# Performance work log

Hardware: AMD Instinct MI355X
Metric: run time of the kernel (lower is better)

The kernel has to match this reference:

```python
import jax, jax.numpy as jnp
import numpy as np

N_NODES = 50000
N_EDGES = 500000
IN_FEATS = 64
HIDDEN = 64
OUT_FEATS = 8
N_LAYERS = 6
NEG_SLOPE = 0.2
LN_EPS = 1e-5


def setup_inputs() -> dict:
    key = jax.random.key(0)
    ks = jax.random.split(key, 12)
    s_in = 1.0 / np.sqrt(IN_FEATS)
    s_h = 1.0 / np.sqrt(HIDDEN)
    return {
        "nodes": jax.random.normal(ks[0], (N_NODES, IN_FEATS), jnp.float32),
        "src": jax.random.randint(ks[1], (N_EDGES,), 0, N_NODES, jnp.int32),
        "dst": jax.random.randint(ks[2], (N_EDGES,), 0, N_NODES, jnp.int32),
        "w_in": jax.random.normal(ks[3], (IN_FEATS, HIDDEN), jnp.float32) * s_in,
        "b_in": jnp.zeros((HIDDEN,), jnp.float32),
        "w_src": jax.random.normal(ks[4], (N_LAYERS, HIDDEN, HIDDEN), jnp.float32) * s_h,
        "b_src": jnp.zeros((N_LAYERS, HIDDEN), jnp.float32),
        "w_dst": jax.random.normal(ks[5], (N_LAYERS, HIDDEN, HIDDEN), jnp.float32) * s_h,
        "b_dst": jnp.zeros((N_LAYERS, HIDDEN), jnp.float32),
        "attn": jax.random.normal(ks[6], (N_LAYERS, HIDDEN), jnp.float32) * s_h,
        "gamma": jnp.ones((N_LAYERS, HIDDEN), jnp.float32),
        "beta": jnp.zeros((N_LAYERS, HIDDEN), jnp.float32),
        "w_out": jax.random.normal(ks[7], (HIDDEN, OUT_FEATS), jnp.float32) * s_h,
        "b_out": jnp.zeros((OUT_FEATS,), jnp.float32),
    }


def _layernorm(x, g, b):
    m = jnp.mean(x, axis=-1, keepdims=True)
    v = jnp.mean(jnp.square(x - m), axis=-1, keepdims=True)
    return (x - m) * jax.lax.rsqrt(v + LN_EPS) * g + b


def _gatv2(h, src, dst, ws, bs, wd, bd, a, n_nodes):
    # GATv2Conv, num_heads=1 (DGL semantics)
    fs = h @ ws + bs                                  # [N, H] fc_src
    fd = h @ wd + bd                                  # [N, H] fc_dst
    e = jax.nn.leaky_relu(fs[src] + fd[dst], NEG_SLOPE)  # [E, H]
    score = e @ a                                     # [E]
    # segment softmax over incoming edges of each dst node
    mx = jax.ops.segment_max(score, dst, num_segments=n_nodes)
    ex = jnp.exp(score - mx[dst])
    denom = jax.ops.segment_sum(ex, dst, num_segments=n_nodes)
    alpha = ex / denom[dst]                           # [E]
    return jax.ops.segment_sum(alpha[:, None] * fs[src], dst, num_segments=n_nodes)


def reference(nodes, src, dst, w_in, b_in, w_src, b_src, w_dst, b_dst, attn, gamma, beta, w_out, b_out):
    n = nodes.shape[0]
    h = nodes @ w_in + b_in
    for i in range(N_LAYERS):
        t = _gatv2(h, src, dst, w_src[i], b_src[i], w_dst[i], b_dst[i], attn[i], n)
        t = _layernorm(t, gamma[i], beta[i])
        h = h + jax.nn.gelu(t, approximate=False)
    return h @ w_out + b_out
```

## Files before the change

kernel.cpp:

```cpp
#include <hip/hip_runtime.h>
#include <math.h>

#define N_NODES 50000
#define N_EDGES 500000
#define NLAYERS 6
#define NEG_SLOPE 0.2f
#define LN_EPS 1e-5f
#define SCAN_B 1024
#define NSCAN_BLOCKS ((N_NODES + SCAN_B - 1) / SCAN_B)
#define LOG2E 1.4426950408889634f

typedef __attribute__((ext_vector_type(8))) short short8;
typedef __attribute__((ext_vector_type(4))) float f32x4;

__device__ __forceinline__ float wave_sum64(float v) {
#pragma unroll
    for (int m = 32; m >= 1; m >>= 1) v += __shfl_xor(v, m, 64);
    return v;
}

__device__ __forceinline__ int wave_incl_scan(int v, int lane) {
#pragma unroll
    for (int offs = 1; offs < 64; offs <<= 1) {
        int t = __shfl_up(v, offs, 64);
        if (lane >= offs) v += t;
    }
    return v;
}

__device__ __forceinline__ unsigned bf16_rne(float v) {
    unsigned u = __float_as_uint(v);
    return (u + 0x7fffu + ((u >> 16) & 1u)) >> 16;
}

__device__ __forceinline__ float fast_exp2(float x) {
    float r;
    asm("v_exp_f32 %0, %1" : "=v"(r) : "v"(x));
    return r;
}

__device__ __forceinline__ float4 bf4_to_f4(ushort4 u) {
    float4 r;
    r.x = __uint_as_float((unsigned)u.x << 16);
    r.y = __uint_as_float((unsigned)u.y << 16);
    r.z = __uint_as_float((unsigned)u.z << 16);
    r.w = __uint_as_float((unsigned)u.w << 16);
    return r;
}

__global__ void count_deg(const int* __restrict__ dst, int* __restrict__ deg,
                          int* __restrict__ hist) {
    if (blockIdx.x == 0 && threadIdx.x < 64) hist[threadIdx.x] = 0;
    int i = blockIdx.x * blockDim.x + threadIdx.x;
    if (i < N_EDGES) atomicAdd(&deg[dst[i]], 1);
}

__global__ void histo(const int* __restrict__ deg, int* __restrict__ hist) {
    __shared__ int lhist[64];
    int t = threadIdx.x;
    if (t < 64) lhist[t] = 0;
    __syncthreads();
    int i = blockIdx.x * SCAN_B + t;
    if (i < N_NODES) atomicAdd(&lhist[min(deg[i], 63)], 1);
    __syncthreads();
    if (t < 64) atomicAdd(&hist[t], lhist[t]);
}

__global__ void binscan(const int* __restrict__ hist, int* __restrict__ binpos) {
    int lane = threadIdx.x;
    int v = hist[lane];
    int incl = wave_incl_scan(v, lane);
    binpos[lane] = incl - v;
}

__global__ void bucket_nodes(const int* __restrict__ deg, int* __restrict__ binpos,
                             int* __restrict__ perm, int* __restrict__ inv_perm) {
    __shared__ int lhist[64], lbase[64];
    int t = threadIdx.x;
    if (t < 64) lhist[t] = 0;
    __syncthreads();
    int i = blockIdx.x * SCAN_B + t;
    int b = 0;
    if (i < N_NODES) {
        b = min(deg[i], 63);
        atomicAdd(&lhist[b], 1);
    }
    __syncthreads();
    if (t < 64) {
        lbase[t] = atomicAdd(&binpos[t], lhist[t]);
        lhist[t] = 0;
    }
    __syncthreads();
    if (i < N_NODES) {
        int r = atomicAdd(&lhist[b], 1);
        int p = lbase[b] + r;
        perm[p] = i;
        inv_perm[i] = p;
    }
}

__global__ void scan1p(const int* __restrict__ deg, const int* __restrict__ perm,
                       int* __restrict__ row_ptr_p, int* __restrict__ bsum) {
    __shared__ int wtot[16];
    int t = threadIdx.x;
    int i = blockIdx.x * SCAN_B + t;
    int lane = t & 63, wv = t >> 6;
    int v = (i < N_NODES) ? deg[perm[i]] : 0;
    int incl = wave_incl_scan(v, lane);
    if (lane == 63) wtot[wv] = incl;
    __syncthreads();
    if (wv == 0) {
        int wval = (lane < 16) ? wtot[lane] : 0;
        int ws = wave_incl_scan(wval, lane);
        if (lane < 16) wtot[lane] = ws - wval;
    }
    __syncthreads();
    int excl = incl - v + wtot[wv];
    if (i < N_NODES) row_ptr_p[i] = excl;
    if (t == SCAN_B - 1) bsum[blockIdx.x] = excl + v;
}

__global__ void scan3p(int* __restrict__ row_ptr_p, const int* __restrict__ bsum,
                       int* __restrict__ pos_p) {
    __shared__ int boff_s;
    int t = threadIdx.x;
    if (t < 64) {
        int v = (t < NSCAN_BLOCKS && t < (int)blockIdx.x) ? bsum[t] : 0;
#pragma unroll
        for (int m = 32; m >= 1; m >>= 1) v += __shfl_xor(v, m, 64);
        if (t == 0) boff_s = v;
    }
    __syncthreads();
    int i = blockIdx.x * SCAN_B + t;
    if (i < N_NODES) {
        int r = row_ptr_p[i] + boff_s;
        row_ptr_p[i] = r;
        pos_p[i] = r;
    }
    if (i == 0) row_ptr_p[N_NODES] = N_EDGES;
}

__global__ void scatter_edges(const int* __restrict__ dst, const int* __restrict__ src,
                              const int* __restrict__ inv_perm, int* __restrict__ pos_p,
                              int* __restrict__ srcs_p) {
    int i = blockIdx.x * blockDim.x + threadIdx.x;
    if (i < N_EDGES) {
        int dp = inv_perm[dst[i]];
        int p = atomicAdd(&pos_p[dp], 1);
        srcs_p[p] = inv_perm[src[i]];
    }
}

__global__ void pack_w(const float* __restrict__ w_in, const float* __restrict__ w_src,
                       const float* __restrict__ w_dst, unsigned short* __restrict__ wpk_hi,
                       unsigned short* __restrict__ wpk_lo) {
    int b = blockIdx.x;
    const float* W = (b == 0) ? w_in
                              : (b <= 6 ? w_src + (size_t)(b - 1) * 4096
                                        : w_dst + (size_t)(b - 7) * 4096);
    unsigned short* hi = wpk_hi + (size_t)b * 4096;
    unsigned short* lo = wpk_lo + (size_t)b * 4096;
    for (int idx = threadIdx.x; idx < 4096; idx += 256) {
        int t = idx >> 10;
        int s = (idx >> 9) & 1;
        int l = (idx >> 3) & 63;
        int j = idx & 7;
        int row = s * 32 + (l >> 4) * 8 + j;
        int col = t * 16 + (l & 15);
        float v = W[row * 64 + col];
        unsigned rh = bf16_rne(v);
        float hf = __uint_as_float(rh << 16);
        unsigned rl = bf16_rne(v - hf);
        hi[idx] = (unsigned short)rh;
        lo[idx] = (unsigned short)rl;
    }
}

__device__ __forceinline__ void load_split8(const float* __restrict__ p, short8& hi, short8& lo) {
    float4 x0 = *(const float4*)p;
    float4 x1 = *(const float4*)(p + 4);
    float v[8] = {x0.x, x0.y, x0.z, x0.w, x1.x, x1.y, x1.z, x1.w};
#pragma unroll
    for (int j = 0; j < 8; ++j) {
        unsigned rh = bf16_rne(v[j]);
        float hf = __uint_as_float(rh << 16);
        unsigned rl = bf16_rne(v[j] - hf);
        hi[j] = (short)rh;
        lo[j] = (short)rl;
    }
}

__device__ __forceinline__ void mfma_16rows(const short8 ah0, const short8 ah1, const short8 al0,
                                            const short8 al1,
                                            const unsigned short* __restrict__ whi,
                                            const unsigned short* __restrict__ wlo, int lane,
                                            f32x4 acc[4]) {
#pragma unroll
    for (int t = 0; t < 4; ++t) {
#pragma unroll
        for (int s = 0; s < 2; ++s) {
            const size_t boff = ((size_t)((t * 2 + s) * 64 + lane)) * 8;
            short8 bh = *(const short8*)(whi + boff);
            short8 bl = *(const short8*)(wlo + boff);
            short8 a_h = s ? ah1 : ah0;
            short8 a_l = s ? al1 : al0;
            acc[t] = __builtin_amdgcn_mfma_f32_16x16x32_bf16(a_h, bh, acc[t], 0, 0, 0);
            acc[t] = __builtin_amdgcn_mfma_f32_16x16x32_bf16(a_l, bh, acc[t], 0, 0, 0);
            acc[t] = __builtin_amdgcn_mfma_f32_16x16x32_bf16(a_h, bl, acc[t], 0, 0, 0);
        }
    }
}

__global__ void mfma_in_proj(const float* __restrict__ X, const int* __restrict__ perm,
                             const unsigned short* __restrict__ whi,
                             const unsigned short* __restrict__ wlo,
                             const float* __restrict__ bias, float* __restrict__ H) {
    int lane = threadIdx.x & 63, wv = threadIdx.x >> 6;
    int R = blockIdx.x * 64 + wv * 16;
    int arow = perm[min(R + (lane & 15), N_NODES - 1)];
    const float* p = X + (size_t)arow * 64 + (lane >> 4) * 8;
    short8 ah0, ah1, al0, al1;
    load_split8(p, ah0, al0);
    load_split8(p + 32, ah1, al1);
    f32x4 acc[4];
    f32x4 z = {0.f, 0.f, 0.f, 0.f};
#pragma unroll
    for (int t = 0; t < 4; ++t) acc[t] = z;
    mfma_16rows(ah0, ah1, al0, al1, whi, wlo, lane, acc);
    int crow = R + (lane >> 4) * 4;
#pragma unroll
    for (int t = 0; t < 4; ++t) {
        int col = t * 16 + (lane & 15);
        float bv = bias[col];
#pragma unroll
        for (int r = 0; r < 4; ++r) {
            int row = crow + r;
            if (row < N_NODES) H[(size_t)row * 64 + col] = acc[t][r] + bv;
        }
    }
}

__global__ void mfma_dual(const float* __restrict__ X, const unsigned short* __restrict__ wshi,
                          const unsigned short* __restrict__ wslo, const float* __restrict__ bs,
                          const unsigned short* __restrict__ wdhi,
                          const unsigned short* __restrict__ wdlo, const float* __restrict__ bd,
                          unsigned short* __restrict__ FS, float* __restrict__ FD) {
    int lane = threadIdx.x & 63, wv = threadIdx.x >> 6;
    int R = blockIdx.x * 64 + wv * 16;
    int arow = min(R + (lane & 15), N_NODES - 1);
    const float* p = X + (size_t)arow * 64 + (lane >> 4) * 8;
    short8 ah0, ah1, al0, al1;
    load_split8(p, ah0, al0);
    load_split8(p + 32, ah1, al1);
    f32x4 accS[4], accD[4];
    f32x4 z = {0.f, 0.f, 0.f, 0.f};
#pragma unroll
    for (int t = 0; t < 4; ++t) {
        accS[t] = z;
        accD[t] = z;
    }
    mfma_16rows(ah0, ah1, al0, al1, wshi, wslo, lane, accS);
    mfma_16rows(ah0, ah1, al0, al1, wdhi, wdlo, lane, accD);
    int crow = R + (lane >> 4) * 4;
#pragma unroll
    for (int t = 0; t < 4; ++t) {
        int col = t * 16 + (lane & 15);
        float bsv = bs[col], bdv = bd[col];
#pragma unroll
        for (int r = 0; r < 4; ++r) {
            int row = crow + r;
            if (row < N_NODES) {
                FS[(size_t)row * 64 + col] = (unsigned short)bf16_rne(accS[t][r] + bsv);
                FD[(size_t)row * 64 + col] = accD[t][r] + bdv;
            }
        }
    }
}

#define WPB 4
__global__ void node_fused_kernel(const unsigned short* __restrict__ fs,
                                  const float* __restrict__ fd, const int* __restrict__ row_ptr,
                                  const int* __restrict__ srcs, const float* __restrict__ attn,
                                  const float* __restrict__ gamma, const float* __restrict__ beta,
                                  float* __restrict__ h) {
    __shared__ float xpose[WPB][64];
    int lane = threadIdx.x & 63;
    int wv = threadIdx.x >> 6;
    int q = lane >> 4;
    int ql = lane & 15;
    int f0 = ql << 2;
    int n = blockIdx.x * WPB + wv;
    if (n >= N_NODES) return;
    float gL = gamma[lane], bL = beta[lane];
    float hval = h[(size_t)n * 64 + lane];
    float4 a4 = *(const float4*)&attn[f0];
    a4.x *= LOG2E;
    a4.y *= LOG2E;
    a4.z *= LOG2E;
    a4.w *= LOG2E;
    int beg = row_ptr[n], end = row_ptr[n + 1];
    int deg = end - beg;
    float4 fd4 = *(const float4*)&fd[(size_t)n * 64 + f0];
    float d = 0.f;
    float4 acc = make_float4(0.f, 0.f, 0.f, 0.f);
    for (int c0 = 0; c0 < deg; c0 += 64) {
        int cl = min(64, deg - c0);
        int sv = (lane < cl) ? srcs[beg + c0 + lane] : 0;
        int nt = (cl + 3) >> 2;
        ushort4 rowA = make_ushort4(0, 0, 0, 0), rowB = rowA;
        int sid0 = __shfl(sv, q, 64);
        if (q < cl) rowA = *(const ushort4*)&fs[(size_t)sid0 * 64 + f0];
        int sid1 = __shfl(sv, (4 + q) & 63, 64);
        if (4 + q < cl) rowB = *(const ushort4*)&fs[(size_t)sid1 * 64 + f0];
        for (int t = 0; t < nt; ++t) {
            int eoff = 4 * t + q;
            bool valid = eoff < cl;
            float4 cur = bf4_to_f4(rowA);
            rowA = rowB;
            int e2 = 4 * (t + 2) + q;
            int sid2 = __shfl(sv, e2 & 63, 64);
            if (e2 < cl) rowB = *(const ushort4*)&fs[(size_t)sid2 * 64 + f0];
            float vx = cur.x + fd4.x, vy = cur.y + fd4.y;
            float vz = cur.z + fd4.z, vw = cur.w + fd4.w;
            vx = fmaxf(vx, NEG_SLOPE * vx);
            vy = fmaxf(vy, NEG_SLOPE * vy);
            vz = fmaxf(vz, NEG_SLOPE * vz);
            vw = fmaxf(vw, NEG_SLOPE * vw);
            float sp = fmaf(a4.x, vx, fmaf(a4.y, vy, fmaf(a4.z, vz, a4.w * vw)));
            sp += __shfl_xor(sp, 1, 64);
            sp += __shfl_xor(sp, 2, 64);
            sp += __shfl_xor(sp, 4, 64);
            sp += __shfl_xor(sp, 8, 64);
            float w = valid ? fast_exp2(sp) : 0.f;
            d += w;
            acc.x = fmaf(w, cur.x, acc.x);
            acc.y = fmaf(w, cur.y, acc.y);
            acc.z = fmaf(w, cur.z, acc.z);
            acc.w = fmaf(w, cur.w, acc.w);
        }
    }
    d += __shfl_xor(d, 16, 64);
    d += __shfl_xor(d, 32, 64);
    acc.x += __shfl_xor(acc.x, 16, 64);
    acc.y += __shfl_xor(acc.y, 16, 64);
    acc.z += __shfl_xor(acc.z, 16, 64);
    acc.w += __shfl_xor(acc.w, 16, 64);
    acc.x += __shfl_xor(acc.x, 32, 64);
    acc.y += __shfl_xor(acc.y, 32, 64);
    acc.z += __shfl_xor(acc.z, 32, 64);
    acc.w += __shfl_xor(acc.w, 32, 64);
    float inv = (d > 0.f) ? 1.f / d : 0.f;
    acc.x *= inv;
    acc.y *= inv;
    acc.z *= inv;
    acc.w *= inv;
    if (q == 0) *(float4*)&xpose[wv][f0] = acc;
    float val = xpose[wv][lane];
    float mean = wave_sum64(val) * 0.015625f;
    float dev = val - mean;
    float var = wave_sum64(dev * dev) * 0.015625f;
    float rstd = rsqrtf(var + LN_EPS);
    float tval = fmaf(dev * rstd, gL, bL);
    float g = 0.5f * tval * (1.f + erff(tval * 0.70710678118654752f));
    h[(size_t)n * 64 + lane] = hval + g;
}

__global__ void out_proj_kernel(const float* __restrict__ h, const int* __restrict__ perm,
                                const float* __restrict__ W, const float* __restrict__ b,
                                float* __restrict__ out) {
    __shared__ float Ws[64 * 8];
    __shared__ float bs[8];
    __shared__ float Hs[32][65];
    int t = threadIdx.x;
    for (int i = t; i < 512; i += 256) Ws[i] = W[i];
    if (t < 8) bs[t] = b[t];
    int n0 = blockIdx.x * 32;
    for (int i = t; i < 32 * 64; i += 256) {
        int r = i >> 6, c = i & 63;
        int n = n0 + r;
        Hs[r][c] = (n < N_NODES) ? h[(size_t)n * 64 + c] : 0.f;
    }
    __syncthreads();
    int nl = t >> 3, o = t & 7;
    int n = n0 + nl;
    if (n >= N_NODES) return;
    float acc = bs[o];
#pragma unroll
    for (int k = 0; k < 64; ++k) acc = fmaf(Hs[nl][k], Ws[k * 8 + o], acc);
    out[(size_t)perm[n] * 8 + o] = acc;
}

extern "C" void kernel_launch(void* const* d_in, const int* in_sizes, int n_in,
                              void* d_out, int out_size, void* d_ws, size_t ws_size,
                              hipStream_t stream) {
    const float* nodes = (const float*)d_in[0];
    const int* src = (const int*)d_in[1];
    const int* dst = (const int*)d_in[2];
    const float* w_in = (const float*)d_in[3];
    const float* b_in = (const float*)d_in[4];
    const float* w_src = (const float*)d_in[5];
    const float* b_src = (const float*)d_in[6];
    const float* w_dst = (const float*)d_in[7];
    const float* b_dst = (const float*)d_in[8];
    const float* attn = (const float*)d_in[9];
    const float* gamma = (const float*)d_in[10];
    const float* beta = (const float*)d_in[11];
    const float* w_out = (const float*)d_in[12];
    const float* b_out = (const float*)d_in[13];
    float* out = (float*)d_out;

    char* ws = (char*)d_ws;
    size_t off = 0;
    auto alloc = [&](size_t bytes) {
        void* p = ws + off;
        off += (bytes + 255) & ~(size_t)255;
        return p;
    };
    float* h = (float*)alloc((size_t)N_NODES * 64 * 4);
    unsigned short* fs = (unsigned short*)alloc((size_t)N_NODES * 64 * 2);
    float* fd = (float*)alloc((size_t)N_NODES * 64 * 4);
    unsigned short* wpk_hi = (unsigned short*)alloc((size_t)13 * 4096 * 2);
    unsigned short* wpk_lo = (unsigned short*)alloc((size_t)13 * 4096 * 2);
    int* deg = (int*)alloc((size_t)N_NODES * 4);
    int* row_ptr_p = (int*)alloc((size_t)(N_NODES + 1) * 4);
    int* pos_p = (int*)alloc((size_t)N_NODES * 4);
    int* srcs_p = (int*)alloc((size_t)N_EDGES * 4);
    int* bsum = (int*)alloc((size_t)NSCAN_BLOCKS * 4);
    int* hist = (int*)alloc((size_t)64 * 4);
    int* binpos = (int*)alloc((size_t)64 * 4);
    int* perm = (int*)alloc((size_t)N_NODES * 4);
    int* inv_perm = (int*)alloc((size_t)N_NODES * 4);

    hipMemsetAsync(deg, 0, (size_t)N_NODES * 4, stream);
    count_deg<<<(N_EDGES + 255) / 256, 256, 0, stream>>>(dst, deg, hist);
    histo<<<NSCAN_BLOCKS, SCAN_B, 0, stream>>>(deg, hist);
    binscan<<<1, 64, 0, stream>>>(hist, binpos);
    bucket_nodes<<<NSCAN_BLOCKS, SCAN_B, 0, stream>>>(deg, binpos, perm, inv_perm);
    scan1p<<<NSCAN_BLOCKS, SCAN_B, 0, stream>>>(deg, perm, row_ptr_p, bsum);
    scan3p<<<NSCAN_BLOCKS, SCAN_B, 0, stream>>>(row_ptr_p, bsum, pos_p);
    scatter_edges<<<(N_EDGES + 255) / 256, 256, 0, stream>>>(dst, src, inv_perm, pos_p, srcs_p);

    pack_w<<<13, 256, 0, stream>>>(w_in, w_src, w_dst, wpk_hi, wpk_lo);

    mfma_in_proj<<<(N_NODES + 63) / 64, 256, 0, stream>>>(nodes, perm, wpk_hi, wpk_lo, b_in, h);

    for (int l = 0; l < NLAYERS; ++l) {
        mfma_dual<<<(N_NODES + 63) / 64, 256, 0, stream>>>(
            h, wpk_hi + (size_t)(1 + l) * 4096, wpk_lo + (size_t)(1 + l) * 4096,
            b_src + (size_t)l * 64, wpk_hi + (size_t)(7 + l) * 4096,
            wpk_lo + (size_t)(7 + l) * 4096, b_dst + (size_t)l * 64, fs, fd);
        node_fused_kernel<<<(N_NODES + WPB - 1) / WPB, 256, 0, stream>>>(
            fs, fd, row_ptr_p, srcs_p, attn + (size_t)l * 64, gamma + (size_t)l * 64,
            beta + (size_t)l * 64, h);
    }

    out_proj_kernel<<<(N_NODES + 31) / 32, 256, 0, stream>>>(h, perm, w_out, b_out, out);
}
```

Before: 346.7 us.

## Fuse graph preprocessing kernels into one cooperative grid-synced kernel

Replaces the memset, degree count, histogram, bucket sort, two-pass scan, edge scatter and weight packing kernels with a single cooperative kernel. Phases are separated by grid-wide syncs and the per-element loops become grid-stride loops over a 49-block grid. This is meant to remove several kernel launches and the idle gaps between them. In exchange, the edge-wide atomic phases run with fewer threads and every phase pays for a grid barrier.

```diff
diff --git a/kernel.cpp b/kernel.cpp
--- a/kernel.cpp
+++ b/kernel.cpp
@@ -1,5 +1,8 @@
 #include <hip/hip_runtime.h>
+#include <hip/hip_cooperative_groups.h>
 #include <math.h>
+
+namespace cg = cooperative_groups;
 
 #define N_NODES 50000
 #define N_EDGES 500000
@@ -48,131 +51,119 @@
     return r;
 }
 
-__global__ void count_deg(const int* __restrict__ dst, int* __restrict__ deg,
-                          int* __restrict__ hist) {
-    if (blockIdx.x == 0 && threadIdx.x < 64) hist[threadIdx.x] = 0;
-    int i = blockIdx.x * blockDim.x + threadIdx.x;
-    if (i < N_EDGES) atomicAdd(&deg[dst[i]], 1);
-}
-
-__global__ void histo(const int* __restrict__ deg, int* __restrict__ hist) {
-    __shared__ int lhist[64];
-    int t = threadIdx.x;
-    if (t < 64) lhist[t] = 0;
-    __syncthreads();
-    int i = blockIdx.x * SCAN_B + t;
-    if (i < N_NODES) atomicAdd(&lhist[min(deg[i], 63)], 1);
-    __syncthreads();
-    if (t < 64) atomicAdd(&hist[t], lhist[t]);
-}
-
-__global__ void binscan(const int* __restrict__ hist, int* __restrict__ binpos) {
-    int lane = threadIdx.x;
-    int v = hist[lane];
-    int incl = wave_incl_scan(v, lane);
-    binpos[lane] = incl - v;
-}
-
-__global__ void bucket_nodes(const int* __restrict__ deg, int* __restrict__ binpos,
-                             int* __restrict__ perm, int* __restrict__ inv_perm) {
-    __shared__ int lhist[64], lbase[64];
-    int t = threadIdx.x;
-    if (t < 64) lhist[t] = 0;
-    __syncthreads();
-    int i = blockIdx.x * SCAN_B + t;
-    int b = 0;
-    if (i < N_NODES) {
-        b = min(deg[i], 63);
-        atomicAdd(&lhist[b], 1);
-    }
-    __syncthreads();
-    if (t < 64) {
-        lbase[t] = atomicAdd(&binpos[t], lhist[t]);
-        lhist[t] = 0;
-    }
-    __syncthreads();
-    if (i < N_NODES) {
-        int r = atomicAdd(&lhist[b], 1);
-        int p = lbase[b] + r;
-        perm[p] = i;
-        inv_perm[i] = p;
-    }
-}
-
-__global__ void scan1p(const int* __restrict__ deg, const int* __restrict__ perm,
-                       int* __restrict__ row_ptr_p, int* __restrict__ bsum) {
-    __shared__ int wtot[16];
-    int t = threadIdx.x;
-    int i = blockIdx.x * SCAN_B + t;
-    int lane = t & 63, wv = t >> 6;
-    int v = (i < N_NODES) ? deg[perm[i]] : 0;
-    int incl = wave_incl_scan(v, lane);
-    if (lane == 63) wtot[wv] = incl;
-    __syncthreads();
-    if (wv == 0) {
-        int wval = (lane < 16) ? wtot[lane] : 0;
-        int ws = wave_incl_scan(wval, lane);
-        if (lane < 16) wtot[lane] = ws - wval;
-    }
-    __syncthreads();
-    int excl = incl - v + wtot[wv];
-    if (i < N_NODES) row_ptr_p[i] = excl;
-    if (t == SCAN_B - 1) bsum[blockIdx.x] = excl + v;
-}
-
-__global__ void scan3p(int* __restrict__ row_ptr_p, const int* __restrict__ bsum,
-                       int* __restrict__ pos_p) {
+__global__ void __launch_bounds__(SCAN_B) build_all(
+    const int* __restrict__ dst, const int* __restrict__ src, const float* __restrict__ w_in,
+    const float* __restrict__ w_src, const float* __restrict__ w_dst,
+    unsigned short* __restrict__ wpk_hi, unsigned short* __restrict__ wpk_lo,
+    int* __restrict__ deg, int* __restrict__ hist, int* __restrict__ binpos,
+    int* __restrict__ perm, int* __restrict__ inv_perm, int* __restrict__ row_ptr_p,
+    int* __restrict__ pos_p, int* __restrict__ srcs_p, int* __restrict__ bsum) {
+    cg::grid_group grid = cg::this_grid();
+    __shared__ int lhist[64], lbase[64], wtot[16];
     __shared__ int boff_s;
-    int t = threadIdx.x;
-    if (t < 64) {
-        int v = (t < NSCAN_BLOCKS && t < (int)blockIdx.x) ? bsum[t] : 0;
-#pragma unroll
-        for (int m = 32; m >= 1; m >>= 1) v += __shfl_xor(v, m, 64);
-        if (t == 0) boff_s = v;
-    }
-    __syncthreads();
-    int i = blockIdx.x * SCAN_B + t;
-    if (i < N_NODES) {
-        int r = row_ptr_p[i] + boff_s;
-        row_ptr_p[i] = r;
-        pos_p[i] = r;
-    }
-    if (i == 0) row_ptr_p[N_NODES] = N_EDGES;
-}
-
-__global__ void scatter_edges(const int* __restrict__ dst, const int* __restrict__ src,
-                              const int* __restrict__ inv_perm, int* __restrict__ pos_p,
-                              int* __restrict__ srcs_p) {
-    int i = blockIdx.x * blockDim.x + threadIdx.x;
-    if (i < N_EDGES) {
-        int dp = inv_perm[dst[i]];
-        int p = atomicAdd(&pos_p[dp], 1);
-        srcs_p[p] = inv_perm[src[i]];
-    }
-}
-
-__global__ void pack_w(const float* __restrict__ w_in, const float* __restrict__ w_src,
-                       const float* __restrict__ w_dst, unsigned short* __restrict__ wpk_hi,
-                       unsigned short* __restrict__ wpk_lo) {
-    int b = blockIdx.x;
-    const float* W = (b == 0) ? w_in
-                              : (b <= 6 ? w_src + (size_t)(b - 1) * 4096
-                                        : w_dst + (size_t)(b - 7) * 4096);
-    unsigned short* hi = wpk_hi + (size_t)b * 4096;
-    unsigned short* lo = wpk_lo + (size_t)b * 4096;
-    for (int idx = threadIdx.x; idx < 4096; idx += 256) {
-        int t = idx >> 10;
-        int s = (idx >> 9) & 1;
-        int l = (idx >> 3) & 63;
-        int j = idx & 7;
+    const int t = threadIdx.x;
+    const int bid = blockIdx.x;
+    const int gtid = bid * SCAN_B + t;
+    const int GSZ = NSCAN_BLOCKS * SCAN_B;
+
+    for (int i = gtid; i < N_NODES; i += GSZ) deg[i] = 0;
+    if (gtid < 64) hist[gtid] = 0;
+    for (int idx = gtid; idx < 13 * 4096; idx += GSZ) {
+        int b = idx >> 12;
+        int k = idx & 4095;
+        const float* W = (b == 0) ? w_in
+                                  : (b <= 6 ? w_src + (size_t)(b - 1) * 4096
+                                            : w_dst + (size_t)(b - 7) * 4096);
+        int tt = k >> 10;
+        int s = (k >> 9) & 1;
+        int l = (k >> 3) & 63;
+        int j = k & 7;
         int row = s * 32 + (l >> 4) * 8 + j;
-        int col = t * 16 + (l & 15);
+        int col = tt * 16 + (l & 15);
         float v = W[row * 64 + col];
         unsigned rh = bf16_rne(v);
         float hf = __uint_as_float(rh << 16);
         unsigned rl = bf16_rne(v - hf);
-        hi[idx] = (unsigned short)rh;
-        lo[idx] = (unsigned short)rl;
+        wpk_hi[(size_t)b * 4096 + k] = (unsigned short)rh;
+        wpk_lo[(size_t)b * 4096 + k] = (unsigned short)rl;
+    }
+    grid.sync();
+
+    for (int i = gtid; i < N_EDGES; i += GSZ) atomicAdd(&deg[dst[i]], 1);
+    grid.sync();
+
+    if (t < 64) lhist[t] = 0;
+    __syncthreads();
+    if (gtid < N_NODES) atomicAdd(&lhist[min(deg[gtid], 63)], 1);
+    __syncthreads();
+    if (t < 64) atomicAdd(&hist[t], lhist[t]);
+    grid.sync();
+
+    if (bid == 0 && t < 64) {
+        int v = hist[t];
+        int incl = wave_incl_scan(v, t);
+        binpos[t] = incl - v;
+    }
+    grid.sync();
+
+    if (t < 64) lhist[t] = 0;
+    __syncthreads();
+    int bkt = 0;
+    if (gtid < N_NODES) {
+        bkt = min(deg[gtid], 63);
+        atomicAdd(&lhist[bkt], 1);
+    }
+    __syncthreads();
+    if (t < 64) {
+        lbase[t] = atomicAdd(&binpos[t], lhist[t]);
+        lhist[t] = 0;
+    }
+    __syncthreads();
+    if (gtid < N_NODES) {
+        int r = atomicAdd(&lhist[bkt], 1);
+        int p = lbase[bkt] + r;
+        perm[p] = gtid;
+        inv_perm[gtid] = p;
+    }
+    grid.sync();
+
+    {
+        int lane = t & 63, wv = t >> 6;
+        int v = (gtid < N_NODES) ? deg[perm[gtid]] : 0;
+        int incl = wave_incl_scan(v, lane);
+        if (lane == 63) wtot[wv] = incl;
+        __syncthreads();
+        if (wv == 0) {
+            int wval = (lane < 16) ? wtot[lane] : 0;
+            int ws = wave_incl_scan(wval, lane);
+            if (lane < 16) wtot[lane] = ws - wval;
+        }
+        __syncthreads();
+        int excl = incl - v + wtot[wv];
+        if (gtid < N_NODES) row_ptr_p[gtid] = excl;
+        if (t == SCAN_B - 1) bsum[bid] = excl + v;
+    }
+    grid.sync();
+
+    if (t < 64) {
+        int v = (t < NSCAN_BLOCKS && t < bid) ? bsum[t] : 0;
+#pragma unroll
+        for (int m = 32; m >= 1; m >>= 1) v += __shfl_xor(v, m, 64);
+        if (t == 0) boff_s = v;
+    }
+    __syncthreads();
+    if (gtid < N_NODES) {
+        int r = row_ptr_p[gtid] + boff_s;
+        row_ptr_p[gtid] = r;
+        pos_p[gtid] = r;
+    }
+    if (gtid == 0) row_ptr_p[N_NODES] = N_EDGES;
+    grid.sync();
+
+    for (int i = gtid; i < N_EDGES; i += GSZ) {
+        int dp = inv_perm[dst[i]];
+        int p = atomicAdd(&pos_p[dp], 1);
+        srcs_p[p] = inv_perm[src[i]];
     }
 }
 
@@ -431,16 +422,14 @@
     int* perm = (int*)alloc((size_t)N_NODES * 4);
     int* inv_perm = (int*)alloc((size_t)N_NODES * 4);
 
-    hipMemsetAsync(deg, 0, (size_t)N_NODES * 4, stream);
-    count_deg<<<(N_EDGES + 255) / 256, 256, 0, stream>>>(dst, deg, hist);
-    histo<<<NSCAN_BLOCKS, SCAN_B, 0, stream>>>(deg, hist);
-    binscan<<<1, 64, 0, stream>>>(hist, binpos);
-    bucket_nodes<<<NSCAN_BLOCKS, SCAN_B, 0, stream>>>(deg, binpos, perm, inv_perm);
-    scan1p<<<NSCAN_BLOCKS, SCAN_B, 0, stream>>>(deg, perm, row_ptr_p, bsum);
-    scan3p<<<NSCAN_BLOCKS, SCAN_B, 0, stream>>>(row_ptr_p, bsum, pos_p);
-    scatter_edges<<<(N_EDGES + 255) / 256, 256, 0, stream>>>(dst, src, inv_perm, pos_p, srcs_p);
-
-    pack_w<<<13, 256, 0, stream>>>(w_in, w_src, w_dst, wpk_hi, wpk_lo);
+    {
+        void* args[] = {(void*)&dst,    (void*)&src,    (void*)&w_in,     (void*)&w_src,
+                        (void*)&w_dst,  (void*)&wpk_hi, (void*)&wpk_lo,   (void*)&deg,
+                        (void*)&hist,   (void*)&binpos, (void*)&perm,     (void*)&inv_perm,
+                        (void*)&row_ptr_p, (void*)&pos_p, (void*)&srcs_p, (void*)&bsum};
+        hipLaunchCooperativeKernel((const void*)build_all, dim3(NSCAN_BLOCKS), dim3(SCAN_B),
+                                   args, 0, stream);
+    }
 
     mfma_in_proj<<<(N_NODES + 63) / 64, 256, 0, stream>>>(nodes, perm, wpk_hi, wpk_lo, b_in, h);
 
```

New measurement: 419.8 us. +21.1%, slower.

## Fuse next-layer src/dst projections into node kernel and input projection

Applied to the files above, without the earlier changes.

Removes the separate per-layer mfma_dual kernel. The input projection now also computes layer-0 FS/FD through a shared-memory transpose. Each node_fused_kernel wave computes the next layer's FS/FD for its single node using MFMA with 15 of 16 rows zeroed, writing into double-buffered fs/fd arrays. This cuts six kernel launches and the re-read of h, at the cost of heavily wasted MFMA work (one useful row per 16) and extra register pressure in the gather kernel.

```diff
diff --git a/kernel.cpp b/kernel.cpp
--- a/kernel.cpp
+++ b/kernel.cpp
@@ -176,7 +176,7 @@
     }
 }
 
-__device__ __forceinline__ void load_split8(const float* __restrict__ p, short8& hi, short8& lo) {
+__device__ __forceinline__ void load_split8(const float* p, short8& hi, short8& lo) {
     float4 x0 = *(const float4*)p;
     float4 x1 = *(const float4*)(p + 4);
     float v[8] = {x0.x, x0.y, x0.z, x0.w, x1.x, x1.y, x1.z, x1.w};
@@ -214,7 +214,15 @@
 __global__ void mfma_in_proj(const float* __restrict__ X, const int* __restrict__ perm,
                              const unsigned short* __restrict__ whi,
                              const unsigned short* __restrict__ wlo,
-                             const float* __restrict__ bias, float* __restrict__ H) {
+                             const float* __restrict__ bias, float* __restrict__ H,
+                             const unsigned short* __restrict__ wshi,
+                             const unsigned short* __restrict__ wslo,
+                             const float* __restrict__ bs,
+                             const unsigned short* __restrict__ wdhi,
+                             const unsigned short* __restrict__ wdlo,
+                             const float* __restrict__ bd, unsigned short* __restrict__ FS,
+                             float* __restrict__ FD) {
+    __shared__ float tr[4][16 * 64];
     int lane = threadIdx.x & 63, wv = threadIdx.x >> 6;
     int R = blockIdx.x * 64 + wv * 16;
     int arow = perm[min(R + (lane & 15), N_NODES - 1)];
@@ -228,6 +236,7 @@
     for (int t = 0; t < 4; ++t) acc[t] = z;
     mfma_16rows(ah0, ah1, al0, al1, whi, wlo, lane, acc);
     int crow = R + (lane >> 4) * 4;
+    int lrow0 = (lane >> 4) * 4;
 #pragma unroll
     for (int t = 0; t < 4; ++t) {
         int col = t * 16 + (lane & 15);
@@ -235,25 +244,14 @@
 #pragma unroll
         for (int r = 0; r < 4; ++r) {
             int row = crow + r;
-            if (row < N_NODES) H[(size_t)row * 64 + col] = acc[t][r] + bv;
-        }
-    }
-}
-
-__global__ void mfma_dual(const float* __restrict__ X, const unsigned short* __restrict__ wshi,
-                          const unsigned short* __restrict__ wslo, const float* __restrict__ bs,
-                          const unsigned short* __restrict__ wdhi,
-                          const unsigned short* __restrict__ wdlo, const float* __restrict__ bd,
-                          unsigned short* __restrict__ FS, float* __restrict__ FD) {
-    int lane = threadIdx.x & 63, wv = threadIdx.x >> 6;
-    int R = blockIdx.x * 64 + wv * 16;
-    int arow = min(R + (lane & 15), N_NODES - 1);
-    const float* p = X + (size_t)arow * 64 + (lane >> 4) * 8;
-    short8 ah0, ah1, al0, al1;
-    load_split8(p, ah0, al0);
-    load_split8(p + 32, ah1, al1);
+            float v = acc[t][r] + bv;
+            if (row < N_NODES) H[(size_t)row * 64 + col] = v;
+            tr[wv][(lrow0 + r) * 64 + col] = v;
+        }
+    }
+    load_split8(&tr[wv][(lane & 15) * 64 + (lane >> 4) * 8], ah0, al0);
+    load_split8(&tr[wv][(lane & 15) * 64 + 32 + (lane >> 4) * 8], ah1, al1);
     f32x4 accS[4], accD[4];
-    f32x4 z = {0.f, 0.f, 0.f, 0.f};
 #pragma unroll
     for (int t = 0; t < 4; ++t) {
         accS[t] = z;
@@ -261,7 +259,6 @@
     }
     mfma_16rows(ah0, ah1, al0, al1, wshi, wslo, lane, accS);
     mfma_16rows(ah0, ah1, al0, al1, wdhi, wdlo, lane, accD);
-    int crow = R + (lane >> 4) * 4;
 #pragma unroll
     for (int t = 0; t < 4; ++t) {
         int col = t * 16 + (lane & 15);
@@ -282,7 +279,14 @@
                                   const float* __restrict__ fd, const int* __restrict__ row_ptr,
                                   const int* __restrict__ srcs, const float* __restrict__ attn,
                                   const float* __restrict__ gamma, const float* __restrict__ beta,
-                                  float* __restrict__ h) {
+                                  float* __restrict__ h,
+                                  const unsigned short* __restrict__ nws_hi,
+                                  const unsigned short* __restrict__ nws_lo,
+                                  const float* __restrict__ nbs,
+                                  const unsigned short* __restrict__ nwd_hi,
+                                  const unsigned short* __restrict__ nwd_lo,
+                                  const float* __restrict__ nbd,
+                                  unsigned short* __restrict__ nFS, float* __restrict__ nFD) {
     __shared__ float xpose[WPB][64];
     int lane = threadIdx.x & 63;
     int wv = threadIdx.x >> 6;
@@ -362,7 +366,38 @@
     float rstd = rsqrtf(var + LN_EPS);
     float tval = fmaf(dev * rstd, gL, bL);
     float g = 0.5f * tval * (1.f + erff(tval * 0.70710678118654752f));
-    h[(size_t)n * 64 + lane] = hval + g;
+    float hnew = hval + g;
+    h[(size_t)n * 64 + lane] = hnew;
+    if (nws_hi) {
+        xpose[wv][lane] = hnew;
+        short8 ah0, ah1, al0, al1;
+        load_split8(&xpose[wv][(lane >> 4) * 8], ah0, al0);
+        load_split8(&xpose[wv][32 + (lane >> 4) * 8], ah1, al1);
+        if (lane & 15) {
+            const short8 s8z = {0, 0, 0, 0, 0, 0, 0, 0};
+            ah0 = s8z;
+            ah1 = s8z;
+            al0 = s8z;
+            al1 = s8z;
+        }
+        f32x4 accS[4], accD[4];
+        f32x4 z4 = {0.f, 0.f, 0.f, 0.f};
+#pragma unroll
+        for (int t = 0; t < 4; ++t) {
+            accS[t] = z4;
+            accD[t] = z4;
+        }
+        mfma_16rows(ah0, ah1, al0, al1, nws_hi, nws_lo, lane, accS);
+        mfma_16rows(ah0, ah1, al0, al1, nwd_hi, nwd_lo, lane, accD);
+        if (lane < 16) {
+#pragma unroll
+            for (int t = 0; t < 4; ++t) {
+                int col = t * 16 + lane;
+                nFS[(size_t)n * 64 + col] = (unsigned short)bf16_rne(accS[t][0] + nbs[col]);
+                nFD[(size_t)n * 64 + col] = accD[t][0] + nbd[col];
+            }
+        }
+    }
 }
 
 __global__ void out_proj_kernel(const float* __restrict__ h, const int* __restrict__ perm,
@@ -417,8 +452,12 @@
         return p;
     };
     float* h = (float*)alloc((size_t)N_NODES * 64 * 4);
-    unsigned short* fs = (unsigned short*)alloc((size_t)N_NODES * 64 * 2);
-    float* fd = (float*)alloc((size_t)N_NODES * 64 * 4);
+    unsigned short* fsbuf[2];
+    float* fdbuf[2];
+    fsbuf[0] = (unsigned short*)alloc((size_t)N_NODES * 64 * 2);
+    fsbuf[1] = (unsigned short*)alloc((size_t)N_NODES * 64 * 2);
+    fdbuf[0] = (float*)alloc((size_t)N_NODES * 64 * 4);
+    fdbuf[1] = (float*)alloc((size_t)N_NODES * 64 * 4);
     unsigned short* wpk_hi = (unsigned short*)alloc((size_t)13 * 4096 * 2);
     unsigned short* wpk_lo = (unsigned short*)alloc((size_t)13 * 4096 * 2);
     int* deg = (int*)alloc((size_t)N_NODES * 4);
@@ -442,16 +481,23 @@
 
     pack_w<<<13, 256, 0, stream>>>(w_in, w_src, w_dst, wpk_hi, wpk_lo);
 
-    mfma_in_proj<<<(N_NODES + 63) / 64, 256, 0, stream>>>(nodes, perm, wpk_hi, wpk_lo, b_in, h);
+    mfma_in_proj<<<(N_NODES + 63) / 64, 256, 0, stream>>>(
+        nodes, perm, wpk_hi, wpk_lo, b_in, h, wpk_hi + (size_t)1 * 4096,
+        wpk_lo + (size_t)1 * 4096, b_src, wpk_hi + (size_t)7 * 4096, wpk_lo + (size_t)7 * 4096,
+        b_dst, fsbuf[0], fdbuf[0]);
 
     for (int l = 0; l < NLAYERS; ++l) {
-        mfma_dual<<<(N_NODES + 63) / 64, 256, 0, stream>>>(
-            h, wpk_hi + (size_t)(1 + l) * 4096, wpk_lo + (size_t)(1 + l) * 4096,
-            b_src + (size_t)l * 64, wpk_hi + (size_t)(7 + l) * 4096,
-            wpk_lo + (size_t)(7 + l) * 4096, b_dst + (size_t)l * 64, fs, fd);
+        bool hasNext = (l + 1) < NLAYERS;
+        const unsigned short* nws_hi = hasNext ? wpk_hi + (size_t)(2 + l) * 4096 : nullptr;
+        const unsigned short* nws_lo = hasNext ? wpk_lo + (size_t)(2 + l) * 4096 : nullptr;
+        const float* nbs = hasNext ? b_src + (size_t)(l + 1) * 64 : nullptr;
+        const unsigned short* nwd_hi = hasNext ? wpk_hi + (size_t)(8 + l) * 4096 : nullptr;
+        const unsigned short* nwd_lo = hasNext ? wpk_lo + (size_t)(8 + l) * 4096 : nullptr;
+        const float* nbd = hasNext ? b_dst + (size_t)(l + 1) * 64 : nullptr;
         node_fused_kernel<<<(N_NODES + WPB - 1) / WPB, 256, 0, stream>>>(
-            fs, fd, row_ptr_p, srcs_p, attn + (size_t)l * 64, gamma + (size_t)l * 64,
-            beta + (size_t)l * 64, h);
+            fsbuf[l & 1], fdbuf[l & 1], row_ptr_p, srcs_p, attn + (size_t)l * 64,
+            gamma + (size_t)l * 64, beta + (size_t)l * 64, h, nws_hi, nws_lo, nbs, nwd_hi,
+            nwd_lo, nbd, fsbuf[(l + 1) & 1], fdbuf[(l + 1) & 1]);
     }
 
     out_proj_kernel<<<(N_NODES + 31) / 32, 256, 0, stream>>>(h, perm, w_out, b_out, out);
```

After: 515.7 us. +48.8%, slower.
